# Kernel optimization log

Measured on AMD Instinct MI355X. Metric: run time of the kernel, lower is better.

The kernel has to match this reference:

```python
import jax, jax.numpy as jnp
import numpy as np

B, S, D, H = 4, 2048, 1024, 16
d = D // H
SCALE = d ** -0.5


def setup_inputs() -> dict:
    key = jax.random.key(0)
    k1, k2, k3 = jax.random.split(key, 3)
    x = jax.random.normal(k1, (B, S, D), dtype=jnp.float32)
    # causal keep-mask (True = keep), shape (B, 1, S, S)
    causal = jnp.tril(jnp.ones((S, S), dtype=bool))
    mask = jnp.broadcast_to(causal[None, None, :, :], (B, 1, S, S))
    # nn.Linear(D, 3D, bias=False): weight (3D, D); out_proj weight (D, D)
    w_qkv = jax.random.normal(k2, (3 * D, D), dtype=jnp.float32) * (D ** -0.5)
    w_out = jax.random.normal(k3, (D, D), dtype=jnp.float32) * (D ** -0.5)
    return {"x": x, "mask": mask, "w_qkv": w_qkv, "w_out": w_out}


def reference(x, mask, w_qkv, w_out):
    # qkv projection: y = x @ W^T, split into q, k, v
    qkv = jnp.einsum('bsd,ed->bse', x, w_qkv)  # (B, S, 3D)
    q, k, v = jnp.split(qkv, 3, axis=-1)
    # (B, S, H, d) -> (B, H, S, d)
    q = q.reshape(B, S, H, d).transpose(0, 2, 1, 3)
    k = k.reshape(B, S, H, d).transpose(0, 2, 1, 3)
    v = v.reshape(B, S, H, d).transpose(0, 2, 1, 3)
    # scores (B, H, S, S)
    attn = jnp.einsum('bhqd,bhkd->bhqk', q, k) * SCALE
    attn = jnp.where(mask, attn, -jnp.inf)
    attn = jax.nn.softmax(attn, axis=-1)
    out = jnp.einsum('bhqk,bhkd->bhqd', attn, v)
    out = out.transpose(0, 2, 1, 3).reshape(B, S, D)
    out = jnp.einsum('bsd,ed->bse', out, w_out)
    return out, (k, v)
```

## Files before the change

kernel.cpp:

```cpp
#include <hip/hip_runtime.h>
#include <hip/hip_bf16.h>

typedef __bf16 bf16_t;
typedef bf16_t bf16x8 __attribute__((ext_vector_type(8)));
typedef bf16_t bf16x4 __attribute__((ext_vector_type(4)));
typedef float  f32x4  __attribute__((ext_vector_type(4)));
typedef float  f32x8  __attribute__((ext_vector_type(8)));
typedef float  f32x16 __attribute__((ext_vector_type(16)));

#define B_  4
#define S_  2048
#define D_  1024
#define H_  16
#define HD  64

#define QSCALE 0.1803368801111204f

#define KV_TILE_ELEMS 4096
#define KV_BH_ELEMS   262144

#define BM 256
#define BN 128
#define BK 64

__device__ __forceinline__ void async_copy16(const void* g, void* l) {
    __builtin_amdgcn_global_load_lds((const __attribute__((address_space(1))) void*)g,
                                     (__attribute__((address_space(3))) void*)l,
                                     16, 0, 0);
}

__device__ __forceinline__ float fast_exp2(float x) {
    float r;
    asm("v_exp_f32 %0, %1" : "=v"(r) : "v"(x));
    return r;
}

__global__ __launch_bounds__(256) void cvt_kernel(const float* __restrict__ in,
                                                  bf16_t* __restrict__ out, int n4) {
    int i = blockIdx.x * 256 + threadIdx.x;
    if (i >= n4) return;
    float4 f = ((const float4*)in)[i];
    bf16x4 o = { (bf16_t)f.x, (bf16_t)f.y, (bf16_t)f.z, (bf16_t)f.w };
    ((bf16x4*)out)[i] = o;
}

__device__ __forceinline__ void gemm_core(const bf16_t* __restrict__ A,
                                          const bf16_t* __restrict__ Bt,
                                          int lda, int ldb, int m0, int n0, int K,
                                          bf16_t* As, bf16_t* Bs, f32x4 acc[4][4]) {
    const int lane = threadIdx.x & 63;
    const int wv   = threadIdx.x >> 6;
    const int wm   = wv >> 1, wn = wv & 1;
    const int r8   = lane >> 3, c8 = lane & 7;
    const int lo   = lane & 15, hi = lane >> 4;
    const int swz  = (lo & 7) * 8;
    const int csw  = (c8 ^ r8) * 8;

    auto stage = [&](int t, int db) {
        const int k0 = t * BK;
        bf16_t* as = As + db * (BM * BK);
        bf16_t* bs = Bs + db * (BN * BK);
        #pragma unroll
        for (int i = 0; i < 4; ++i) {
            const int row = i * 64 + wv * 8 + r8;
            async_copy16(A + (size_t)(m0 + row) * lda + k0 + csw, as + (i * 64 + wv * 8) * BK);
        }
        #pragma unroll
        for (int i = 0; i < 2; ++i) {
            const int row = i * 64 + wv * 8 + r8;
            async_copy16(Bt + (size_t)(n0 + row) * ldb + k0 + csw, bs + (i * 64 + wv * 8) * BK);
        }
    };

    auto compute = [&](int db) {
        const bf16_t* as = As + db * (BM * BK);
        const bf16_t* bs = Bs + db * (BN * BK);
        #pragma unroll
        for (int kk = 0; kk < 2; ++kk) {
            const int kos = (kk * 32 + hi * 8) ^ swz;
            bf16x8 aF[4], bF[4];
            #pragma unroll
            for (int m = 0; m < 4; ++m)
                aF[m] = *(const bf16x8*)(as + (wm * 64 + m * 16 + lo) * BK + kos);
            #pragma unroll
            for (int n = 0; n < 4; ++n)
                bF[n] = *(const bf16x8*)(bs + (wn * 64 + n * 16 + lo) * BK + kos);
            #pragma unroll
            for (int m = 0; m < 4; ++m)
                #pragma unroll
                for (int n = 0; n < 4; ++n)
                    acc[m][n] = __builtin_amdgcn_mfma_f32_16x16x32_bf16(aF[m], bF[n], acc[m][n], 0, 0, 0);
        }
    };

    const int nt = K / BK;
    stage(0, 0); stage(1, 1); stage(2, 2);

    for (int t = 0; t < nt; ++t) {
        const int db = t % 3;
        if (t + 2 < nt)      asm volatile("s_waitcnt vmcnt(12)" ::: "memory");
        else if (t + 1 < nt) asm volatile("s_waitcnt vmcnt(6)"  ::: "memory");
        else                 asm volatile("s_waitcnt vmcnt(0)"  ::: "memory");
        __builtin_amdgcn_s_barrier();
        __builtin_amdgcn_sched_barrier(0);
        compute(db);
        __builtin_amdgcn_sched_barrier(0);
        __builtin_amdgcn_s_barrier();
        __builtin_amdgcn_sched_barrier(0);
        if (t + 3 < nt) stage(t + 3, db);
    }
}

__global__ __launch_bounds__(512) void gemm_qkv_kernel(const bf16_t* __restrict__ A,
                                                       const bf16_t* __restrict__ Bt,
                                                       float* __restrict__ out,
                                                       bf16_t* __restrict__ q_ws,
                                                       bf16_t* __restrict__ kv_frag) {
    __shared__ __align__(16) bf16_t As[3 * BM * BK];
    __shared__ __align__(16) bf16_t Bs[3 * BN * BK];
    const int m0 = blockIdx.y * BM, n0 = blockIdx.x * BN;
    f32x4 acc[4][4];
    #pragma unroll
    for (int m = 0; m < 4; ++m)
        #pragma unroll
        for (int n = 0; n < 4; ++n) acc[m][n] = f32x4{0.f, 0.f, 0.f, 0.f};

    gemm_core(A, Bt, D_, D_, m0, n0, D_, As, Bs, acc);

    const int lane = threadIdx.x & 63, wv = threadIdx.x >> 6;
    const int wm = wv >> 1, wn = wv & 1;
    const int lo = lane & 15, hi = lane >> 4;
    #pragma unroll
    for (int m = 0; m < 4; ++m) {
        #pragma unroll
        for (int n = 0; n < 4; ++n) {
            const int gcol = n0 + wn * 64 + n * 16 + lo;
            const int sec  = gcol >> 10;
            const int e    = gcol & 1023;
            const int h    = e >> 6, dv = e & 63;
            #pragma unroll
            for (int j4 = 0; j4 < 4; ++j4) {
                const int grow = m0 + wm * 64 + m * 16 + hi * 4 + j4;
                const float v  = acc[m][n][j4];
                const int b = grow >> 11, s = grow & 2047;
                const size_t idx2 = ((((size_t)b * H_ + h) * S_ + s) << 6) + dv;
                if (sec == 0) {
                    q_ws[idx2] = (bf16_t)(v * QSCALE);
                } else if (sec == 1) {
                    out[8388608u + idx2] = v;
                    const int bh   = b * H_ + h;
                    const int tile = s >> 5, ql = s & 31;
                    const int c    = dv >> 4, hb = (dv >> 3) & 1, jj = dv & 7;
                    kv_frag[(((size_t)bh * 64 + tile) * 8 + c) * 512 + hb * 256 + ql * 8 + jj] = (bf16_t)v;
                } else {
                    out[16777216u + idx2] = v;
                }
            }
        }
    }
}

__global__ __launch_bounds__(256) void build_vfrag_kernel(const float* __restrict__ v_f32,
                                                          bf16_t* __restrict__ kv_frag) {
    __shared__ __align__(16) bf16_t T[64][72];
    const int bh = blockIdx.x;
    const int s0 = blockIdx.y * 64;
    const int t  = threadIdx.x;
    {
        const int sl  = t >> 2;
        const int dv0 = (t & 3) * 16;
        const float* src = v_f32 + ((size_t)bh * S_ + s0 + sl) * HD + dv0;
        float tmp[16];
        #pragma unroll
        for (int i = 0; i < 4; ++i) *(float4*)(tmp + i * 4) = ((const float4*)src)[i];
        #pragma unroll
        for (int i = 0; i < 16; ++i) T[dv0 + i][sl] = (bf16_t)tmp[i];
    }
    __syncthreads();
    {
        const int st = t >> 7;
        const int r  = t & 127;
        const int cc = r >> 5;
        const int l  = r & 31;
        const int khi = cc >> 1, hd = cc & 1;
        const int d   = hd * 32 + l;
        const int tile = (s0 >> 5) + st;
        bf16_t* dst = kv_frag + (((size_t)bh * 64 + tile) * 8 + 4 + cc) * 512 + l * 8;
        const int slb = st * 32 + khi * 16;
        *(bf16x8*)(dst)       = *(const bf16x8*)&T[d][slb];
        *(bf16x8*)(dst + 256) = *(const bf16x8*)&T[d][slb + 8];
    }
}

__global__ __launch_bounds__(256) void attn_kernel(const bf16_t* __restrict__ q_ws,
                                                   const bf16_t* __restrict__ kv_frag,
                                                   bf16_t* __restrict__ attn_ws) {
    __shared__ __align__(16) float MRG[2][2][64][20];
    __shared__ float LSUM[2][64];
    __shared__ __align__(16) bf16_t T[2][32][72];
    const int lane = threadIdx.x & 63;
    const int wv   = threadIdx.x >> 6;
    const int blk   = blockIdx.x;
    const int x     = blk & 7;
    const int r     = blk >> 3;
    const int bh    = x + 8 * (r & 7);
    const int pr    = wv >> 1;
    const int khalf = wv & 1;
    const int p     = (r >> 3) * 2 + pr;

    const int ql = lane & 31;
    const int hb = lane >> 5;
    const size_t kv_base = (size_t)bh * (S_ * HD);
    const int b = bh >> 4, h = bh & 15;

    const bf16_t* kvb = kv_frag + (size_t)bh * KV_BH_ELEMS + (size_t)lane * 8;

    auto load_k = [&](int tile, bf16x8 kf[4]) {
        const bf16_t* tp = kvb + (size_t)tile * KV_TILE_ELEMS;
        #pragma unroll
        for (int c = 0; c < 4; ++c) kf[c] = *(const bf16x8*)(tp + c * 512);
    };
    auto load_v = [&](int tile, bf16x8 vf[4]) {
        const bf16_t* tp = kvb + (size_t)tile * KV_TILE_ELEMS + 2048;
        #pragma unroll
        for (int i = 0; i < 4; ++i) vf[i] = *(const bf16x8*)(tp + i * 512);
    };

    #pragma unroll 1
    for (int pass = 0; pass < 2; ++pass) {
        const int qblock = pass ? (63 - p) : p;
        const int q0 = qblock * 32;
        const int nt  = qblock + 1;
        const int mid = nt >> 1;
        const int tstart = khalf ? mid : 0;
        const int tend   = khalf ? nt  : mid;

        bf16x8 qF[4];
        const bf16_t* qrow = q_ws + kv_base + (size_t)(q0 + ql) * HD + hb * 8;
        #pragma unroll
        for (int c = 0; c < 4; ++c) qF[c] = *(const bf16x8*)(qrow + 16 * c);

        f32x16 accT0 = {}, accT1 = {};
        float lsum = 0.f;

        auto compute_tile = [&](const bf16x8 kf[4], const bf16x8 vf[4], bool diag) {
            f32x16 s = {};
            #pragma unroll
            for (int c = 0; c < 4; ++c)
                s = __builtin_amdgcn_mfma_f32_32x32x16_bf16(kf[c], qF[c], s, 0, 0, 0);
            if (diag) {
                #pragma unroll
                for (int rr = 0; rr < 16; ++rr) {
                    const int kloc = (rr & 3) + 8 * (rr >> 2) + 4 * hb;
                    if (kloc > ql) s[rr] = -1e30f;
                }
            }
            #pragma unroll
            for (int rr = 0; rr < 16; ++rr) s[rr] = fast_exp2(s[rr]);
            f32x8 t8 = __builtin_shufflevector(s, s, 0, 1, 2, 3, 4, 5, 6, 7) +
                       __builtin_shufflevector(s, s, 8, 9, 10, 11, 12, 13, 14, 15);
            f32x4 t4 = __builtin_shufflevector(t8, t8, 0, 1, 2, 3) +
                       __builtin_shufflevector(t8, t8, 4, 5, 6, 7);
            lsum += (t4[0] + t4[1]) + (t4[2] + t4[3]);

            unsigned w[8];
            #pragma unroll
            for (int i = 0; i < 8; ++i) {
                unsigned d;
                asm("v_cvt_pk_bf16_f32 %0, %1, %2" : "=v"(d) : "v"(s[2 * i]), "v"(s[2 * i + 1]));
                w[i] = d;
            }
            union { unsigned u[4]; bf16x8 v; } pf0, pf1;
            {
                auto r0 = __builtin_amdgcn_permlane32_swap(w[0], w[2], false, false);
                auto r1 = __builtin_amdgcn_permlane32_swap(w[1], w[3], false, false);
                pf0.u[0] = r0[0]; pf0.u[1] = r1[0]; pf0.u[2] = r0[1]; pf0.u[3] = r1[1];
            }
            {
                auto r0 = __builtin_amdgcn_permlane32_swap(w[4], w[6], false, false);
                auto r1 = __builtin_amdgcn_permlane32_swap(w[5], w[7], false, false);
                pf1.u[0] = r0[0]; pf1.u[1] = r1[0]; pf1.u[2] = r0[1]; pf1.u[3] = r1[1];
            }

            accT0 = __builtin_amdgcn_mfma_f32_32x32x16_bf16(vf[0], pf0.v, accT0, 0, 0, 0);
            accT1 = __builtin_amdgcn_mfma_f32_32x32x16_bf16(vf[1], pf0.v, accT1, 0, 0, 0);
            accT0 = __builtin_amdgcn_mfma_f32_32x32x16_bf16(vf[2], pf1.v, accT0, 0, 0, 0);
            accT1 = __builtin_amdgcn_mfma_f32_32x32x16_bf16(vf[3], pf1.v, accT1, 0, 0, 0);
        };

        int t = tstart;
        for (; t + 1 < tend; t += 2) {
            bf16x8 kA[4], vA[4], kB[4], vB[4];
            load_k(t, kA);
            load_v(t, vA);
            load_k(t + 1, kB);
            load_v(t + 1, vB);
            compute_tile(kA, vA, t == qblock);
            compute_tile(kB, vB, (t + 1) == qblock);
        }
        if (t < tend) {
            bf16x8 kA[4], vA[4];
            load_k(t, kA);
            load_v(t, vA);
            compute_tile(kA, vA, t == qblock);
        }

        if (khalf) {
            *(f32x16*)&MRG[pr][0][lane][0] = accT0;
            *(f32x16*)&MRG[pr][1][lane][0] = accT1;
            LSUM[pr][lane] = lsum;
        }
        __syncthreads();
        if (!khalf) {
            accT0 += *(const f32x16*)&MRG[pr][0][lane][0];
            accT1 += *(const f32x16*)&MRG[pr][1][lane][0];
            lsum  += LSUM[pr][lane];
            const float ltot = lsum + __shfl_xor(lsum, 32, 64);
            const float inv  = 1.0f / ltot;
            #pragma unroll
            for (int rr = 0; rr < 16; ++rr) {
                const int dl = (rr & 3) + 8 * (rr >> 2) + 4 * hb;
                T[pr][ql][dl]      = (bf16_t)(accT0[rr] * inv);
                T[pr][ql][32 + dl] = (bf16_t)(accT1[rr] * inv);
            }
            asm volatile("s_waitcnt lgkmcnt(0)" ::: "memory");
            #pragma unroll
            for (int it = 0; it < 4; ++it) {
                const int ch  = it * 64 + lane;
                const int row = ch >> 3, c8 = ch & 7;
                bf16x8 o = *(const bf16x8*)&T[pr][row][c8 * 8];
                *(bf16x8*)(attn_ws + ((size_t)(b * S_ + q0 + row)) * D_ + h * HD + c8 * 8) = o;
            }
        }
        __syncthreads();
    }
}

__global__ __launch_bounds__(512) void gemm_out_kernel(const bf16_t* __restrict__ A,
                                                       const bf16_t* __restrict__ Bt,
                                                       float* __restrict__ out) {
    __shared__ __align__(16) bf16_t As[3 * BM * BK];
    __shared__ __align__(16) bf16_t Bs[3 * BN * BK];
    const int m0 = blockIdx.y * BM, n0 = blockIdx.x * BN;
    f32x4 acc[4][4];
    #pragma unroll
    for (int m = 0; m < 4; ++m)
        #pragma unroll
        for (int n = 0; n < 4; ++n) acc[m][n] = f32x4{0.f, 0.f, 0.f, 0.f};

    gemm_core(A, Bt, D_, D_, m0, n0, D_, As, Bs, acc);

    const int lane = threadIdx.x & 63, wv = threadIdx.x >> 6;
    const int wm = wv >> 1, wn = wv & 1;
    const int lo = lane & 15, hi = lane >> 4;
    #pragma unroll
    for (int m = 0; m < 4; ++m) {
        #pragma unroll
        for (int n = 0; n < 4; ++n) {
            const int gcol = n0 + wn * 64 + n * 16 + lo;
            #pragma unroll
            for (int j = 0; j < 4; ++j) {
                const int grow = m0 + wm * 64 + m * 16 + hi * 4 + j;
                out[(size_t)grow * D_ + gcol] = acc[m][n][j];
            }
        }
    }
}

extern "C" void kernel_launch(void* const* d_in, const int* in_sizes, int n_in,
                              void* d_out, int out_size, void* d_ws, size_t ws_size,
                              hipStream_t stream) {
    (void)in_sizes; (void)n_in; (void)out_size; (void)ws_size;
    const float* x     = (const float*)d_in[0];
    const float* w_qkv = (const float*)d_in[2];
    const float* w_out = (const float*)d_in[3];
    float* out = (float*)d_out;
    char* ws = (char*)d_ws;

    bf16_t* x_bf    = (bf16_t*)(ws);
    bf16_t* wqkv_bf = (bf16_t*)(ws + 16777216);
    bf16_t* wout_bf = (bf16_t*)(ws + 23068672);
    bf16_t* q_ws    = (bf16_t*)(ws + 25165824);
    bf16_t* kv_frag = (bf16_t*)(ws + 41943040);
    bf16_t* attn_ws = (bf16_t*)(ws + 75497472);

    cvt_kernel<<<8192, 256, 0, stream>>>(x, x_bf, 2097152);
    cvt_kernel<<<3072, 256, 0, stream>>>(w_qkv, wqkv_bf, 786432);
    cvt_kernel<<<1024, 256, 0, stream>>>(w_out, wout_bf, 262144);

    gemm_qkv_kernel<<<dim3(24, 32), 512, 0, stream>>>(x_bf, wqkv_bf, out, q_ws, kv_frag);
    build_vfrag_kernel<<<dim3(64, 32), 256, 0, stream>>>(out + 16777216, kv_frag);
    attn_kernel<<<1024, 256, 0, stream>>>(q_ws, kv_frag, attn_ws);
    gemm_out_kernel<<<dim3(8, 32), 512, 0, stream>>>(attn_ws, wout_bf, out);
}
```

Measured before the change: 184.8 us.

## Rework GEMM core: BK=32 quad-buffered pipeline, 256x256 QKV tiles, earlier prefetch

Replaces the fixed 256x128, BK=64 triple-buffered GEMM core with a templated core that uses BK=32 slices, four LDS buffers and a new swizzle. The next stage is now issued before compute rather than after the trailing barrier. The QKV projection moves to 256x256 tiles with 8x4 MFMA repeats per wave, halving its grid to 384 blocks. This aims for more reuse per loaded tile and better overlap of loads with MFMA work, at the cost of more accumulator registers and fewer blocks, which may leave CUs underfilled.

```diff
diff --git a/kernel.cpp b/kernel.cpp
--- a/kernel.cpp
+++ b/kernel.cpp
@@ -19,10 +19,6 @@
 #define KV_TILE_ELEMS 4096
 #define KV_BH_ELEMS   262144
 
-#define BM 256
-#define BN 128
-#define BK 64
-
 __device__ __forceinline__ void async_copy16(const void* g, void* l) {
     __builtin_amdgcn_global_load_lds((const __attribute__((address_space(1))) void*)g,
                                      (__attribute__((address_space(3))) void*)l,
@@ -33,6 +29,15 @@
     float r;
     asm("v_exp_f32 %0, %1" : "=v"(r) : "v"(x));
     return r;
+}
+
+template<int N>
+__device__ __forceinline__ void wait_vmcnt() {
+    if constexpr (N == 8)      asm volatile("s_waitcnt vmcnt(8)" ::: "memory");
+    else if constexpr (N == 6) asm volatile("s_waitcnt vmcnt(6)" ::: "memory");
+    else if constexpr (N == 4) asm volatile("s_waitcnt vmcnt(4)" ::: "memory");
+    else if constexpr (N == 3) asm volatile("s_waitcnt vmcnt(3)" ::: "memory");
+    else                       asm volatile("s_waitcnt vmcnt(0)" ::: "memory");
 }
 
 __global__ __launch_bounds__(256) void cvt_kernel(const float* __restrict__ in,
@@ -44,70 +49,74 @@
     ((bf16x4*)out)[i] = o;
 }
 
-__device__ __forceinline__ void gemm_core(const bf16_t* __restrict__ A,
-                                          const bf16_t* __restrict__ Bt,
-                                          int lda, int ldb, int m0, int n0, int K,
-                                          bf16_t* As, bf16_t* Bs, f32x4 acc[4][4]) {
+template<int WNS, int MREP, int NREP>
+__device__ __forceinline__ void gemm_core256(const bf16_t* __restrict__ A,
+                                             const bf16_t* __restrict__ Bt,
+                                             int lda, int ldb, int m0, int n0, int K,
+                                             bf16_t* LDS, f32x4 acc[MREP][NREP]) {
+    constexpr int BM   = (8 / WNS) * MREP * 16;
+    constexpr int BN   = WNS * NREP * 16;
+    constexpr int BUFE = (BM + BN) * 32;
+    constexpr int AI   = BM / 128;
+    constexpr int BI   = BN / 128;
+    constexpr int LPS  = AI + BI;
+
     const int lane = threadIdx.x & 63;
     const int wv   = threadIdx.x >> 6;
-    const int wm   = wv >> 1, wn = wv & 1;
-    const int r8   = lane >> 3, c8 = lane & 7;
+    const int wm   = wv / WNS, wn = wv % WNS;
     const int lo   = lane & 15, hi = lane >> 4;
-    const int swz  = (lo & 7) * 8;
-    const int csw  = (c8 ^ r8) * 8;
+    const int srd  = (lo >> 1) & 3;
+    const int r_in = lane >> 2;
+    const int csw  = (((lane & 3) ^ ((lane >> 3) & 3))) * 8;
 
     auto stage = [&](int t, int db) {
-        const int k0 = t * BK;
-        bf16_t* as = As + db * (BM * BK);
-        bf16_t* bs = Bs + db * (BN * BK);
-        #pragma unroll
-        for (int i = 0; i < 4; ++i) {
-            const int row = i * 64 + wv * 8 + r8;
-            async_copy16(A + (size_t)(m0 + row) * lda + k0 + csw, as + (i * 64 + wv * 8) * BK);
-        }
-        #pragma unroll
-        for (int i = 0; i < 2; ++i) {
-            const int row = i * 64 + wv * 8 + r8;
-            async_copy16(Bt + (size_t)(n0 + row) * ldb + k0 + csw, bs + (i * 64 + wv * 8) * BK);
+        const int k0 = t * 32;
+        bf16_t* dstA = LDS + db * BUFE;
+        bf16_t* dstB = dstA + BM * 32;
+        #pragma unroll
+        for (int i = 0; i < AI; ++i) {
+            const int base = wv * (BM / 8) + i * 16;
+            async_copy16(A + (size_t)(m0 + base + r_in) * lda + k0 + csw, dstA + base * 32);
+        }
+        #pragma unroll
+        for (int i = 0; i < BI; ++i) {
+            const int base = wv * (BN / 8) + i * 16;
+            async_copy16(Bt + (size_t)(n0 + base + r_in) * ldb + k0 + csw, dstB + base * 32);
         }
     };
 
     auto compute = [&](int db) {
-        const bf16_t* as = As + db * (BM * BK);
-        const bf16_t* bs = Bs + db * (BN * BK);
-        #pragma unroll
-        for (int kk = 0; kk < 2; ++kk) {
-            const int kos = (kk * 32 + hi * 8) ^ swz;
-            bf16x8 aF[4], bF[4];
-            #pragma unroll
-            for (int m = 0; m < 4; ++m)
-                aF[m] = *(const bf16x8*)(as + (wm * 64 + m * 16 + lo) * BK + kos);
-            #pragma unroll
-            for (int n = 0; n < 4; ++n)
-                bF[n] = *(const bf16x8*)(bs + (wn * 64 + n * 16 + lo) * BK + kos);
-            #pragma unroll
-            for (int m = 0; m < 4; ++m)
-                #pragma unroll
-                for (int n = 0; n < 4; ++n)
-                    acc[m][n] = __builtin_amdgcn_mfma_f32_16x16x32_bf16(aF[m], bF[n], acc[m][n], 0, 0, 0);
-        }
+        const bf16_t* as = LDS + db * BUFE;
+        const bf16_t* bs = as + BM * 32;
+        const int kos = (hi ^ srd) * 8;
+        bf16x8 aF[MREP], bF[NREP];
+        #pragma unroll
+        for (int m = 0; m < MREP; ++m)
+            aF[m] = *(const bf16x8*)(as + (wm * (MREP * 16) + m * 16 + lo) * 32 + kos);
+        #pragma unroll
+        for (int n = 0; n < NREP; ++n)
+            bF[n] = *(const bf16x8*)(bs + (wn * (NREP * 16) + n * 16 + lo) * 32 + kos);
+        #pragma unroll
+        for (int m = 0; m < MREP; ++m)
+            #pragma unroll
+            for (int n = 0; n < NREP; ++n)
+                acc[m][n] = __builtin_amdgcn_mfma_f32_16x16x32_bf16(aF[m], bF[n], acc[m][n], 0, 0, 0);
     };
 
-    const int nt = K / BK;
+    const int nt = K / 32;
     stage(0, 0); stage(1, 1); stage(2, 2);
 
     for (int t = 0; t < nt; ++t) {
-        const int db = t % 3;
-        if (t + 2 < nt)      asm volatile("s_waitcnt vmcnt(12)" ::: "memory");
-        else if (t + 1 < nt) asm volatile("s_waitcnt vmcnt(6)"  ::: "memory");
-        else                 asm volatile("s_waitcnt vmcnt(0)"  ::: "memory");
+        const int db = t & 3;
+        if (t + 2 < nt)      wait_vmcnt<2 * LPS>();
+        else if (t + 1 < nt) wait_vmcnt<LPS>();
+        else                 wait_vmcnt<0>();
         __builtin_amdgcn_s_barrier();
         __builtin_amdgcn_sched_barrier(0);
+        if (t + 3 < nt) stage(t + 3, (t + 3) & 3);
         compute(db);
         __builtin_amdgcn_sched_barrier(0);
         __builtin_amdgcn_s_barrier();
-        __builtin_amdgcn_sched_barrier(0);
-        if (t + 3 < nt) stage(t + 3, db);
     }
 }
 
@@ -116,22 +125,21 @@
                                                        float* __restrict__ out,
                                                        bf16_t* __restrict__ q_ws,
                                                        bf16_t* __restrict__ kv_frag) {
-    __shared__ __align__(16) bf16_t As[3 * BM * BK];
-    __shared__ __align__(16) bf16_t Bs[3 * BN * BK];
-    const int m0 = blockIdx.y * BM, n0 = blockIdx.x * BN;
-    f32x4 acc[4][4];
+    __shared__ __align__(16) bf16_t LDS[4 * (256 + 256) * 32];
+    const int m0 = blockIdx.y * 256, n0 = blockIdx.x * 256;
+    f32x4 acc[8][4];
     #pragma unroll
-    for (int m = 0; m < 4; ++m)
+    for (int m = 0; m < 8; ++m)
         #pragma unroll
         for (int n = 0; n < 4; ++n) acc[m][n] = f32x4{0.f, 0.f, 0.f, 0.f};
 
-    gemm_core(A, Bt, D_, D_, m0, n0, D_, As, Bs, acc);
+    gemm_core256<4, 8, 4>(A, Bt, D_, D_, m0, n0, D_, LDS, acc);
 
     const int lane = threadIdx.x & 63, wv = threadIdx.x >> 6;
-    const int wm = wv >> 1, wn = wv & 1;
+    const int wm = wv >> 2, wn = wv & 3;
     const int lo = lane & 15, hi = lane >> 4;
     #pragma unroll
-    for (int m = 0; m < 4; ++m) {
+    for (int m = 0; m < 8; ++m) {
         #pragma unroll
         for (int n = 0; n < 4; ++n) {
             const int gcol = n0 + wn * 64 + n * 16 + lo;
@@ -140,7 +148,7 @@
             const int h    = e >> 6, dv = e & 63;
             #pragma unroll
             for (int j4 = 0; j4 < 4; ++j4) {
-                const int grow = m0 + wm * 64 + m * 16 + hi * 4 + j4;
+                const int grow = m0 + wm * 128 + m * 16 + hi * 4 + j4;
                 const float v  = acc[m][n][j4];
                 const int b = grow >> 11, s = grow & 2047;
                 const size_t idx2 = ((((size_t)b * H_ + h) * S_ + s) << 6) + dv;
@@ -339,16 +347,15 @@
 __global__ __launch_bounds__(512) void gemm_out_kernel(const bf16_t* __restrict__ A,
                                                        const bf16_t* __restrict__ Bt,
                                                        float* __restrict__ out) {
-    __shared__ __align__(16) bf16_t As[3 * BM * BK];
-    __shared__ __align__(16) bf16_t Bs[3 * BN * BK];
-    const int m0 = blockIdx.y * BM, n0 = blockIdx.x * BN;
+    __shared__ __align__(16) bf16_t LDS[4 * (256 + 128) * 32];
+    const int m0 = blockIdx.y * 256, n0 = blockIdx.x * 128;
     f32x4 acc[4][4];
     #pragma unroll
     for (int m = 0; m < 4; ++m)
         #pragma unroll
         for (int n = 0; n < 4; ++n) acc[m][n] = f32x4{0.f, 0.f, 0.f, 0.f};
 
-    gemm_core(A, Bt, D_, D_, m0, n0, D_, As, Bs, acc);
+    gemm_core256<2, 4, 4>(A, Bt, D_, D_, m0, n0, D_, LDS, acc);
 
     const int lane = threadIdx.x & 63, wv = threadIdx.x >> 6;
     const int wm = wv >> 1, wn = wv & 1;
@@ -388,7 +395,7 @@
     cvt_kernel<<<3072, 256, 0, stream>>>(w_qkv, wqkv_bf, 786432);
     cvt_kernel<<<1024, 256, 0, stream>>>(w_out, wout_bf, 262144);
 
-    gemm_qkv_kernel<<<dim3(24, 32), 512, 0, stream>>>(x_bf, wqkv_bf, out, q_ws, kv_frag);
+    gemm_qkv_kernel<<<dim3(12, 32), 512, 0, stream>>>(x_bf, wqkv_bf, out, q_ws, kv_frag);
     build_vfrag_kernel<<<dim3(64, 32), 256, 0, stream>>>(out + 16777216, kv_frag);
     attn_kernel<<<1024, 256, 0, stream>>>(q_ws, kv_frag, attn_ws);
     gemm_out_kernel<<<dim3(8, 32), 512, 0, stream>>>(attn_ws, wout_bf, out);
```

Result: no change. 184.1 us (-0.4%).
